# Optimization experiments

Measured on AMD Instinct MI355X. Metric: run time of the kernel, lower is better.

Reference implementation:

```python
import jax, jax.numpy as jnp
import numpy as np

N = 50000       # node_num
E = 800000      # edges (no self loops; reference adds them)
IN_C = 128
OUT_C = 128
HEADS = 1
NEG_SLOPE = 0.2
BN_EPS = 1e-5


def setup_inputs() -> dict:
    key = jax.random.key(0)
    ks = jax.random.split(key, 12)
    x = jax.random.normal(ks[0], (N, IN_C), dtype=jnp.float32)
    # edge_index with no self-loops: dst = (src + off) % N, off in [1, N)
    src = jax.random.randint(ks[1], (E,), 0, N)
    off = jax.random.randint(ks[2], (E,), 1, N)
    dst = (src + off) % N
    edge_index = jnp.stack([src, dst]).astype(jnp.int64)
    embedding = jax.random.normal(ks[3], (N, OUT_C), dtype=jnp.float32)
    s = 1.0 / np.sqrt(IN_C)
    lin_w = jax.random.uniform(ks[4], (HEADS * OUT_C, IN_C), jnp.float32, -s, s)
    g = 0.1
    att_i = jax.random.normal(ks[5], (1, HEADS, OUT_C), jnp.float32) * g
    att_j = jax.random.normal(ks[6], (1, HEADS, OUT_C), jnp.float32) * g
    att_em_i = jax.random.normal(ks[7], (1, HEADS, OUT_C), jnp.float32) * g
    att_em_j = jax.random.normal(ks[8], (1, HEADS, OUT_C), jnp.float32) * g
    bias = jnp.zeros((OUT_C,), jnp.float32)
    gamma = jnp.ones((OUT_C,), jnp.float32)
    beta = jnp.zeros((OUT_C,), jnp.float32)
    return {"x": x, "edge_index": edge_index, "embedding": embedding,
            "lin_w": lin_w, "att_i": att_i, "att_j": att_j,
            "att_em_i": att_em_i, "att_em_j": att_em_j,
            "bias": bias, "gamma": gamma, "beta": beta}


def _gnn_forward(x, embedding, lin_w, att_i, att_j, att_em_i, att_em_j,
                 bias, gamma, beta, src, dst):
    n = x.shape[0]
    xl = (x @ lin_w.T).reshape(n, HEADS, OUT_C)          # [N,H,C]
    x_j = xl[src]                                         # [E',H,C] source
    x_i = xl[dst]                                         # [E',H,C] target
    emb_i = embedding[dst][:, None, :]                    # [E',1,C]
    emb_j = embedding[src][:, None, :]
    # alpha_e = <[x_i||emb_i], [att_i||att_em_i]> + <[x_j||emb_j], [att_j||att_em_j]>
    alpha = ((x_i * att_i).sum(-1) + (emb_i * att_em_i).sum(-1)
             + (x_j * att_j).sum(-1) + (emb_j * att_em_j).sum(-1))  # [E',H]
    alpha = jnp.where(alpha >= 0, alpha, NEG_SLOPE * alpha)         # leaky_relu
    # segment softmax over destination node (PyG softmax)
    amax = jax.ops.segment_max(alpha, dst, num_segments=n)
    ex = jnp.exp(alpha - amax[dst])
    denom = jax.ops.segment_sum(ex, dst, num_segments=n)
    alpha = ex / (denom[dst] + 1e-16)                               # [E',H]
    out = jax.ops.segment_sum(x_j * alpha[..., None], dst, num_segments=n)  # [N,H,C]
    out = out.mean(axis=1) + bias                                   # concat=False
    # BatchNorm1d, training mode (biased batch variance)
    mu = out.mean(axis=0)
    var = ((out - mu) ** 2).mean(axis=0)
    return (out - mu) * jax.lax.rsqrt(var + BN_EPS) * gamma + beta


def reference(x, edge_index, embedding, lin_w, att_i, att_j,
              att_em_i, att_em_j, bias, gamma, beta):
    n = x.shape[0]
    loops = jnp.arange(n, dtype=edge_index.dtype)
    src = jnp.concatenate([edge_index[0], loops])
    dst = jnp.concatenate([edge_index[1], loops])
    return _gnn_forward(x, embedding, lin_w, att_i, att_j, att_em_i,
                        att_em_j, bias, gamma, beta, src, dst)
```

## Files before the change

kernel.cpp:

```cpp
#include <hip/hip_runtime.h>

typedef short bf16x8 __attribute__((ext_vector_type(8)));
typedef float f32x4 __attribute__((ext_vector_type(4)));

__device__ __forceinline__ unsigned short f2bf(float f) {
  unsigned int u = __float_as_uint(f);
  u += 0x7fffu + ((u >> 16) & 1u);
  return (unsigned short)(u >> 16);
}
__device__ __forceinline__ float bf2f(unsigned short h) {
  return __uint_as_float(((unsigned int)h) << 16);
}
__device__ __forceinline__ float lrelu(float a) { return a >= 0.f ? a : 0.2f * a; }

__global__ void zero_kernel(int* __restrict__ p, int n) {
  int i = blockIdx.x * blockDim.x + threadIdx.x;
  int stride = gridDim.x * blockDim.x;
  for (; i < n; i += stride) p[i] = 0;
}

__global__ __launch_bounds__(256) void gemm_kernel(
    const float* __restrict__ x, const float* __restrict__ w,
    unsigned short* __restrict__ xl, int n) {
  __shared__ __align__(16) unsigned short xs[64 * 128];
  __shared__ __align__(16) unsigned short wl[128 * 128];
  const int t = threadIdx.x;
  const int r0 = blockIdx.x * 64;
#pragma unroll
  for (int i = 0; i < 16; ++i) {
    int f4 = t + i * 256;
    int row = f4 >> 5;
    int kk = (f4 & 31) << 2;
    float4 v = *(const float4*)(w + row * 128 + kk);
    ushort4 b;
    b.x = f2bf(v.x); b.y = f2bf(v.y); b.z = f2bf(v.z); b.w = f2bf(v.w);
    int boff = (kk << 1) ^ ((row & 7) << 4);
    *(ushort4*)((char*)wl + row * 256 + boff) = b;
  }
#pragma unroll
  for (int i = 0; i < 8; ++i) {
    int f4 = t + i * 256;
    int row = f4 >> 5;
    int kk = (f4 & 31) << 2;
    int gr = r0 + row;
    float4 v;
    if (gr < n) v = *(const float4*)(x + gr * 128 + kk);
    else { v.x = 0.f; v.y = 0.f; v.z = 0.f; v.w = 0.f; }
    ushort4 b;
    b.x = f2bf(v.x); b.y = f2bf(v.y); b.z = f2bf(v.z); b.w = f2bf(v.w);
    int boff = (kk << 1) ^ ((row & 7) << 4);
    *(ushort4*)((char*)xs + row * 256 + boff) = b;
  }
  __syncthreads();
  const int wid = t >> 6, lane = t & 63;
  const int m16 = lane & 15, kg = lane >> 4;
  const int arow = wid * 16 + m16;
  const f32x4 vzero = {0.f, 0.f, 0.f, 0.f};
  f32x4 acc[8];
#pragma unroll
  for (int i = 0; i < 8; ++i) acc[i] = vzero;
#pragma unroll
  for (int s = 0; s < 4; ++s) {
    int kb = s * 64 + kg * 16;
    bf16x8 a = *(const bf16x8*)((const char*)xs + arow * 256 + (kb ^ ((arow & 7) << 4)));
#pragma unroll
    for (int cf = 0; cf < 8; ++cf) {
      int wrow = cf * 16 + m16;
      bf16x8 b = *(const bf16x8*)((const char*)wl + wrow * 256 + (kb ^ ((wrow & 7) << 4)));
      acc[cf] = __builtin_amdgcn_mfma_f32_16x16x32_bf16(a, b, acc[cf], 0, 0, 0);
    }
  }
  const int crow0 = wid * 16 + (lane >> 4) * 4;
#pragma unroll
  for (int q = 0; q < 4; ++q) {
    int gr = r0 + crow0 + q;
    if (gr < n) {
#pragma unroll
      for (int cf = 0; cf < 8; ++cf)
        xl[gr * 128 + cf * 16 + m16] = f2bf(acc[cf][q]);
    }
  }
}

__global__ __launch_bounds__(256) void atts_kernel(
    const unsigned short* __restrict__ xl, const float* __restrict__ emb,
    const float* __restrict__ att_i, const float* __restrict__ att_j,
    const float* __restrict__ att_em_i, const float* __restrict__ att_em_j,
    float* __restrict__ ai, float* __restrict__ aj, int n) {
  int wid = threadIdx.x >> 6, lane = threadIdx.x & 63;
  int node = blockIdx.x * 4 + wid;
  if (node >= n) return;
  int c0 = lane, c1 = lane + 64;
  float x0 = bf2f(xl[node * 128 + c0]);
  float x1 = bf2f(xl[node * 128 + c1]);
  float e0 = emb[node * 128 + c0];
  float e1 = emb[node * 128 + c1];
  float si = x0 * att_i[c0] + x1 * att_i[c1] + e0 * att_em_i[c0] + e1 * att_em_i[c1];
  float sj = x0 * att_j[c0] + x1 * att_j[c1] + e0 * att_em_j[c0] + e1 * att_em_j[c1];
#pragma unroll
  for (int off = 32; off > 0; off >>= 1) {
    si += __shfl_xor(si, off);
    sj += __shfl_xor(sj, off);
  }
  if (lane == 0) { ai[node] = si; aj[node] = sj; }
}

__global__ __launch_bounds__(256) void count_rank_kernel(
    const int* __restrict__ dst, int* __restrict__ cnt, int* __restrict__ pw, int E) {
  int e = (blockIdx.x * blockDim.x + threadIdx.x) * 4;
  if (e + 3 < E) {
    int4 d4 = *(const int4*)(dst + e);
    int4 p4;
    p4.x = atomicAdd(&cnt[d4.x], 1);
    p4.y = atomicAdd(&cnt[d4.y], 1);
    p4.z = atomicAdd(&cnt[d4.z], 1);
    p4.w = atomicAdd(&cnt[d4.w], 1);
    *(int4*)(pw + e) = p4;
  } else {
    for (; e < E; ++e) pw[e] = atomicAdd(&cnt[dst[e]], 1);
  }
}

__global__ __launch_bounds__(1024) void scan1_kernel(
    const int* __restrict__ cnt, int* __restrict__ rp, int* __restrict__ bsum, int n) {
  __shared__ int wsum[16];
  int t = threadIdx.x, lane = t & 63, wid = t >> 6;
  int i = blockIdx.x * 1024 + t;
  int v = (i < n) ? cnt[i] : 0;
  int incl = v;
#pragma unroll
  for (int off = 1; off < 64; off <<= 1) {
    int u = __shfl_up(incl, off);
    if (lane >= off) incl += u;
  }
  if (lane == 63) wsum[wid] = incl;
  __syncthreads();
  if (t < 16) {
    int wv = wsum[t];
    int winc = wv;
#pragma unroll
    for (int off = 1; off < 16; off <<= 1) {
      int u = __shfl_up(winc, off);
      if (t >= off) winc += u;
    }
    wsum[t] = winc - wv;
  }
  __syncthreads();
  int excl = wsum[wid] + incl - v;
  if (i < n) rp[i] = excl;
  if (t == 1023) bsum[blockIdx.x] = excl + v;
}

__global__ __launch_bounds__(64) void scan2_kernel(
    int* __restrict__ bsum, int* __restrict__ rp, int nb, int n) {
  int t = threadIdx.x;
  int carry = 0;
  for (int base = 0; base < nb; base += 64) {
    int idx = base + t;
    int v = (idx < nb) ? bsum[idx] : 0;
    int incl = v;
#pragma unroll
    for (int off = 1; off < 64; off <<= 1) {
      int u = __shfl_up(incl, off);
      if (t >= off) incl += u;
    }
    if (idx < nb) bsum[idx] = carry + incl - v;
    carry += __shfl(incl, 63);
  }
  if (t == 0) rp[n] = carry;
}

__global__ __launch_bounds__(256) void scan3_kernel(
    const int* __restrict__ bsum, int* __restrict__ rp, int n) {
  int i = blockIdx.x * blockDim.x + threadIdx.x;
  if (i < n) rp[i] += bsum[i >> 10];
}

__global__ __launch_bounds__(256) void scatter_kernel(
    const int* __restrict__ src, const int* __restrict__ dst,
    const int* __restrict__ rp, const int* __restrict__ pw,
    int* __restrict__ csr, int E) {
  int e = (blockIdx.x * blockDim.x + threadIdx.x) * 4;
  if (e + 3 < E) {
    int4 s4 = *(const int4*)(src + e);
    int4 d4 = *(const int4*)(dst + e);
    int4 p4 = *(const int4*)(pw + e);
    int r0 = rp[d4.x], r1 = rp[d4.y], r2 = rp[d4.z], r3 = rp[d4.w];
    csr[r0 + p4.x] = s4.x;
    csr[r1 + p4.y] = s4.y;
    csr[r2 + p4.z] = s4.z;
    csr[r3 + p4.w] = s4.w;
  } else {
    for (; e < E; ++e) csr[rp[dst[e]] + pw[e]] = src[e];
  }
}

__global__ __launch_bounds__(256) void agg_kernel(
    const float* __restrict__ ai, const float* __restrict__ aj,
    const unsigned short* __restrict__ xl,
    const int* __restrict__ row_ptr, const int* __restrict__ csr_src,
    const float* __restrict__ bias, float* __restrict__ out, int n) {
  __shared__ float s_we[4][64];
  __shared__ int s_id[4][64];
  int wid = threadIdx.x >> 6, lane = threadIdx.x & 63;
  int node = blockIdx.x * 4 + wid;
  if (node >= n) return;
  int beg = row_ptr[node], end = row_ptr[node + 1];
  float ain = ai[node];
  float a_self = lrelu(ain + aj[node]);
  float m = a_self;
  float dl = 0.f;
  float acc0 = 0.f, acc1 = 0.f;
  const int c0 = lane * 2;
  for (int cs = beg; cs < end; cs += 64) {
    int ce = min(64, end - cs);
    int s = 0;
    float a = -3.4e38f;
    if (lane < ce) {
      s = csr_src[cs + lane];
      a = lrelu(ain + aj[s]);
    }
    float cm = a;
#pragma unroll
    for (int off = 32; off > 0; off >>= 1) cm = fmaxf(cm, __shfl_xor(cm, off));
    float nm = fmaxf(m, cm);
    float scale = __expf(m - nm);
    dl *= scale; acc0 *= scale; acc1 *= scale;
    m = nm;
    float we = (lane < ce) ? __expf(a - nm) : 0.f;
    dl += we;
    s_we[wid][lane] = we;
    s_id[wid][lane] = s;
    int j = 0;
    for (; j + 4 <= ce; j += 4) {
      float w0 = s_we[wid][j],     w1 = s_we[wid][j + 1];
      float w2 = s_we[wid][j + 2], w3 = s_we[wid][j + 3];
      int i0 = s_id[wid][j],     i1 = s_id[wid][j + 1];
      int i2 = s_id[wid][j + 2], i3 = s_id[wid][j + 3];
      ushort2 v0 = *(const ushort2*)(xl + i0 * 128 + c0);
      ushort2 v1 = *(const ushort2*)(xl + i1 * 128 + c0);
      ushort2 v2 = *(const ushort2*)(xl + i2 * 128 + c0);
      ushort2 v3 = *(const ushort2*)(xl + i3 * 128 + c0);
      acc0 += w0 * bf2f(v0.x); acc1 += w0 * bf2f(v0.y);
      acc0 += w1 * bf2f(v1.x); acc1 += w1 * bf2f(v1.y);
      acc0 += w2 * bf2f(v2.x); acc1 += w2 * bf2f(v2.y);
      acc0 += w3 * bf2f(v3.x); acc1 += w3 * bf2f(v3.y);
    }
    for (; j < ce; ++j) {
      float w0 = s_we[wid][j];
      int i0 = s_id[wid][j];
      ushort2 v0 = *(const ushort2*)(xl + i0 * 128 + c0);
      acc0 += w0 * bf2f(v0.x); acc1 += w0 * bf2f(v0.y);
    }
  }
  float w_self = __expf(a_self - m);
#pragma unroll
  for (int off = 32; off > 0; off >>= 1) dl += __shfl_xor(dl, off);
  float inv = 1.f / (dl + w_self + 1e-16f);
  ushort2 u = *(const ushort2*)(xl + node * 128 + c0);
  float2 o;
  o.x = (acc0 + w_self * bf2f(u.x)) * inv + bias[c0];
  o.y = (acc1 + w_self * bf2f(u.y)) * inv + bias[c0 + 1];
  *(float2*)(out + node * 128 + c0) = o;
}

__global__ __launch_bounds__(256) void bnstat_kernel(
    const float* __restrict__ out, float* __restrict__ sums,
    float* __restrict__ sumsq, int n) {
  int c = threadIdx.x & 127;
  int half = threadIdx.x >> 7;
  float s = 0.f, q = 0.f;
  for (int r = blockIdx.x * 2 + half; r < n; r += gridDim.x * 2) {
    float v = out[r * 128 + c];
    s += v;
    q += v * v;
  }
  atomicAdd(&sums[c], s);
  atomicAdd(&sumsq[c], q);
}

__global__ __launch_bounds__(256) void bnapply_kernel(
    float* __restrict__ out, const float* __restrict__ sums,
    const float* __restrict__ sumsq, const float* __restrict__ gamma,
    const float* __restrict__ beta, int n, float invN) {
  int total = n * 128;
  int i = blockIdx.x * blockDim.x + threadIdx.x;
  int stride = gridDim.x * blockDim.x;
  for (; i < total; i += stride) {
    int c = i & 127;
    float mu = sums[c] * invN;
    float var = sumsq[c] * invN - mu * mu;
    out[i] = (out[i] - mu) * rsqrtf(var + 1e-5f) * gamma[c] + beta[c];
  }
}

extern "C" void kernel_launch(void* const* d_in, const int* in_sizes, int n_in,
                              void* d_out, int out_size, void* d_ws, size_t ws_size,
                              hipStream_t stream) {
  (void)n_in; (void)out_size; (void)ws_size;
  const float* x = (const float*)d_in[0];
  const int* ei = (const int*)d_in[1];
  const float* emb = (const float*)d_in[2];
  const float* lin_w = (const float*)d_in[3];
  const float* att_i = (const float*)d_in[4];
  const float* att_j = (const float*)d_in[5];
  const float* att_em_i = (const float*)d_in[6];
  const float* att_em_j = (const float*)d_in[7];
  const float* bias = (const float*)d_in[8];
  const float* gamma = (const float*)d_in[9];
  const float* beta = (const float*)d_in[10];
  float* out = (float*)d_out;
  const int N = in_sizes[0] / 128;
  const int E = in_sizes[1] / 2;
  const int* src = ei;
  const int* dst = ei + E;
  const int NB = (N + 1023) / 1024;

  auto align_up = [](size_t v) { return (v + 255) & ~(size_t)255; };
  size_t off = 0;
  size_t xl_off = off;    off = align_up(off + (size_t)N * 128 * 2);
  size_t ai_off = off;    off = align_up(off + (size_t)N * 4);
  size_t aj_off = off;    off = align_up(off + (size_t)N * 4);
  size_t rp_off = off;    off = align_up(off + (size_t)(N + 1) * 4);
  size_t csr_off = off;   off = align_up(off + (size_t)E * 4);
  size_t pw_off = off;    off = align_up(off + (size_t)E * 4);
  size_t bsum_off = off;  off = align_up(off + (size_t)(NB + 1) * 4);
  size_t cnt_off = off;   off = align_up(off + (size_t)N * 4);
  size_t sums_off = off;  off = align_up(off + 512);
  size_t sumsq_off = off; off = align_up(off + 512);
  size_t end_off = off;

  char* ws = (char*)d_ws;
  unsigned short* xl = (unsigned short*)(ws + xl_off);
  float* ai = (float*)(ws + ai_off);
  float* aj = (float*)(ws + aj_off);
  int* rp = (int*)(ws + rp_off);
  int* csr = (int*)(ws + csr_off);
  int* pw = (int*)(ws + pw_off);
  int* bsum = (int*)(ws + bsum_off);
  int* cnt = (int*)(ws + cnt_off);
  float* sums = (float*)(ws + sums_off);
  float* sumsq = (float*)(ws + sumsq_off);

  int zwords = (int)((end_off - cnt_off) / 4);
  hipLaunchKernelGGL(zero_kernel, dim3((zwords + 255) / 256), dim3(256), 0, stream,
                     cnt, zwords);
  hipLaunchKernelGGL(gemm_kernel, dim3((N + 63) / 64), dim3(256), 0, stream,
                     x, lin_w, xl, N);
  hipLaunchKernelGGL(atts_kernel, dim3((N + 3) / 4), dim3(256), 0, stream,
                     xl, emb, att_i, att_j, att_em_i, att_em_j, ai, aj, N);
  hipLaunchKernelGGL(count_rank_kernel, dim3((E / 4 + 255) / 256), dim3(256), 0, stream,
                     dst, cnt, pw, E);
  hipLaunchKernelGGL(scan1_kernel, dim3(NB), dim3(1024), 0, stream, cnt, rp, bsum, N);
  hipLaunchKernelGGL(scan2_kernel, dim3(1), dim3(64), 0, stream, bsum, rp, NB, N);
  hipLaunchKernelGGL(scan3_kernel, dim3((N + 255) / 256), dim3(256), 0, stream,
                     bsum, rp, N);
  hipLaunchKernelGGL(scatter_kernel, dim3((E / 4 + 255) / 256), dim3(256), 0, stream,
                     src, dst, rp, pw, csr, E);
  hipLaunchKernelGGL(agg_kernel, dim3((N + 3) / 4), dim3(256), 0, stream,
                     ai, aj, xl, rp, csr, bias, out, N);
  hipLaunchKernelGGL(bnstat_kernel, dim3(256), dim3(256), 0, stream,
                     out, sums, sumsq, N);
  hipLaunchKernelGGL(bnapply_kernel, dim3(2048), dim3(256), 0, stream,
                     out, sums, sumsq, gamma, beta, N, 1.0f / (float)N);
}
```

Before: 262.8 us.

## Fuse attention scores into GEMM, drop softmax max, vectorize BN kernels

Several changes at once. The per-node attention dot products move into the GEMM epilogue, computed from the MFMA accumulators plus a vectorized embedding read, which removes the separate atts kernel and its reread of xl. The aggregation kernel drops the online running-max softmax and exponentiates the raw leaky-relu scores. It also passes edge weights and indices through wave shuffles instead of LDS and unrolls the gather by 8. The BatchNorm stat and apply kernels switch to float4 accesses, with a block-level LDS reduction and precomputed scale and shift. Skipping the max subtraction risks exp overflow when attention logits are large.

```diff
diff --git a/kernel.cpp b/kernel.cpp
--- a/kernel.cpp
+++ b/kernel.cpp
@@ -21,7 +21,11 @@
 
 __global__ __launch_bounds__(256) void gemm_kernel(
     const float* __restrict__ x, const float* __restrict__ w,
-    unsigned short* __restrict__ xl, int n) {
+    const float* __restrict__ emb,
+    const float* __restrict__ att_i, const float* __restrict__ att_j,
+    const float* __restrict__ att_em_i, const float* __restrict__ att_em_j,
+    unsigned short* __restrict__ xl, float* __restrict__ ai, float* __restrict__ aj,
+    int n) {
   __shared__ __align__(16) unsigned short xs[64 * 128];
   __shared__ __align__(16) unsigned short wl[128 * 128];
   const int t = threadIdx.x;
@@ -70,7 +74,7 @@
       acc[cf] = __builtin_amdgcn_mfma_f32_16x16x32_bf16(a, b, acc[cf], 0, 0, 0);
     }
   }
-  const int crow0 = wid * 16 + (lane >> 4) * 4;
+  const int crow0 = wid * 16 + kg * 4;
 #pragma unroll
   for (int q = 0; q < 4; ++q) {
     int gr = r0 + crow0 + q;
@@ -80,29 +84,41 @@
         xl[gr * 128 + cf * 16 + m16] = f2bf(acc[cf][q]);
     }
   }
-}
-
-__global__ __launch_bounds__(256) void atts_kernel(
-    const unsigned short* __restrict__ xl, const float* __restrict__ emb,
-    const float* __restrict__ att_i, const float* __restrict__ att_j,
-    const float* __restrict__ att_em_i, const float* __restrict__ att_em_j,
-    float* __restrict__ ai, float* __restrict__ aj, int n) {
-  int wid = threadIdx.x >> 6, lane = threadIdx.x & 63;
-  int node = blockIdx.x * 4 + wid;
-  if (node >= n) return;
-  int c0 = lane, c1 = lane + 64;
-  float x0 = bf2f(xl[node * 128 + c0]);
-  float x1 = bf2f(xl[node * 128 + c1]);
-  float e0 = emb[node * 128 + c0];
-  float e1 = emb[node * 128 + c1];
-  float si = x0 * att_i[c0] + x1 * att_i[c1] + e0 * att_em_i[c0] + e1 * att_em_i[c1];
-  float sj = x0 * att_j[c0] + x1 * att_j[c1] + e0 * att_em_j[c0] + e1 * att_em_j[c1];
-#pragma unroll
-  for (int off = 32; off > 0; off >>= 1) {
-    si += __shfl_xor(si, off);
-    sj += __shfl_xor(sj, off);
-  }
-  if (lane == 0) { ai[node] = si; aj[node] = sj; }
+  float ati[8], atj[8];
+#pragma unroll
+  for (int cf = 0; cf < 8; ++cf) {
+    ati[cf] = att_i[cf * 16 + m16];
+    atj[cf] = att_j[cf * 16 + m16];
+  }
+  float4 aemi0 = *(const float4*)(att_em_i + m16 * 8);
+  float4 aemi1 = *(const float4*)(att_em_i + m16 * 8 + 4);
+  float4 aemj0 = *(const float4*)(att_em_j + m16 * 8);
+  float4 aemj1 = *(const float4*)(att_em_j + m16 * 8 + 4);
+#pragma unroll
+  for (int q = 0; q < 4; ++q) {
+    int gr = r0 + crow0 + q;
+    if (gr < n) {
+      float si = 0.f, sj = 0.f;
+#pragma unroll
+      for (int cf = 0; cf < 8; ++cf) {
+        si += acc[cf][q] * ati[cf];
+        sj += acc[cf][q] * atj[cf];
+      }
+      const float* ep = emb + (size_t)gr * 128 + m16 * 8;
+      float4 e0 = *(const float4*)(ep);
+      float4 e1 = *(const float4*)(ep + 4);
+      si += e0.x * aemi0.x + e0.y * aemi0.y + e0.z * aemi0.z + e0.w * aemi0.w
+          + e1.x * aemi1.x + e1.y * aemi1.y + e1.z * aemi1.z + e1.w * aemi1.w;
+      sj += e0.x * aemj0.x + e0.y * aemj0.y + e0.z * aemj0.z + e0.w * aemj0.w
+          + e1.x * aemj1.x + e1.y * aemj1.y + e1.z * aemj1.z + e1.w * aemj1.w;
+#pragma unroll
+      for (int off = 1; off < 16; off <<= 1) {
+        si += __shfl_xor(si, off);
+        sj += __shfl_xor(sj, off);
+      }
+      if (m16 == 0) { ai[gr] = si; aj[gr] = sj; }
+    }
+  }
 }
 
 __global__ __launch_bounds__(256) void count_rank_kernel(
@@ -200,97 +216,129 @@
     const unsigned short* __restrict__ xl,
     const int* __restrict__ row_ptr, const int* __restrict__ csr_src,
     const float* __restrict__ bias, float* __restrict__ out, int n) {
-  __shared__ float s_we[4][64];
-  __shared__ int s_id[4][64];
   int wid = threadIdx.x >> 6, lane = threadIdx.x & 63;
   int node = blockIdx.x * 4 + wid;
   if (node >= n) return;
   int beg = row_ptr[node], end = row_ptr[node + 1];
   float ain = ai[node];
-  float a_self = lrelu(ain + aj[node]);
-  float m = a_self;
+  float w_self = __expf(lrelu(ain + aj[node]));
   float dl = 0.f;
   float acc0 = 0.f, acc1 = 0.f;
   const int c0 = lane * 2;
   for (int cs = beg; cs < end; cs += 64) {
     int ce = min(64, end - cs);
     int s = 0;
-    float a = -3.4e38f;
+    float we = 0.f;
     if (lane < ce) {
       s = csr_src[cs + lane];
-      a = lrelu(ain + aj[s]);
-    }
-    float cm = a;
-#pragma unroll
-    for (int off = 32; off > 0; off >>= 1) cm = fmaxf(cm, __shfl_xor(cm, off));
-    float nm = fmaxf(m, cm);
-    float scale = __expf(m - nm);
-    dl *= scale; acc0 *= scale; acc1 *= scale;
-    m = nm;
-    float we = (lane < ce) ? __expf(a - nm) : 0.f;
+      we = __expf(lrelu(ain + aj[s]));
+    }
     dl += we;
-    s_we[wid][lane] = we;
-    s_id[wid][lane] = s;
     int j = 0;
-    for (; j + 4 <= ce; j += 4) {
-      float w0 = s_we[wid][j],     w1 = s_we[wid][j + 1];
-      float w2 = s_we[wid][j + 2], w3 = s_we[wid][j + 3];
-      int i0 = s_id[wid][j],     i1 = s_id[wid][j + 1];
-      int i2 = s_id[wid][j + 2], i3 = s_id[wid][j + 3];
-      ushort2 v0 = *(const ushort2*)(xl + i0 * 128 + c0);
-      ushort2 v1 = *(const ushort2*)(xl + i1 * 128 + c0);
-      ushort2 v2 = *(const ushort2*)(xl + i2 * 128 + c0);
-      ushort2 v3 = *(const ushort2*)(xl + i3 * 128 + c0);
+    for (; j + 8 <= ce; j += 8) {
+      float w0 = __shfl(we, j),     w1 = __shfl(we, j + 1);
+      float w2 = __shfl(we, j + 2), w3 = __shfl(we, j + 3);
+      float w4 = __shfl(we, j + 4), w5 = __shfl(we, j + 5);
+      float w6 = __shfl(we, j + 6), w7 = __shfl(we, j + 7);
+      int i0 = __shfl(s, j),     i1 = __shfl(s, j + 1);
+      int i2 = __shfl(s, j + 2), i3 = __shfl(s, j + 3);
+      int i4 = __shfl(s, j + 4), i5 = __shfl(s, j + 5);
+      int i6 = __shfl(s, j + 6), i7 = __shfl(s, j + 7);
+      ushort2 v0 = *(const ushort2*)(xl + (size_t)i0 * 128 + c0);
+      ushort2 v1 = *(const ushort2*)(xl + (size_t)i1 * 128 + c0);
+      ushort2 v2 = *(const ushort2*)(xl + (size_t)i2 * 128 + c0);
+      ushort2 v3 = *(const ushort2*)(xl + (size_t)i3 * 128 + c0);
+      ushort2 v4 = *(const ushort2*)(xl + (size_t)i4 * 128 + c0);
+      ushort2 v5 = *(const ushort2*)(xl + (size_t)i5 * 128 + c0);
+      ushort2 v6 = *(const ushort2*)(xl + (size_t)i6 * 128 + c0);
+      ushort2 v7 = *(const ushort2*)(xl + (size_t)i7 * 128 + c0);
       acc0 += w0 * bf2f(v0.x); acc1 += w0 * bf2f(v0.y);
       acc0 += w1 * bf2f(v1.x); acc1 += w1 * bf2f(v1.y);
       acc0 += w2 * bf2f(v2.x); acc1 += w2 * bf2f(v2.y);
       acc0 += w3 * bf2f(v3.x); acc1 += w3 * bf2f(v3.y);
+      acc0 += w4 * bf2f(v4.x); acc1 += w4 * bf2f(v4.y);
+      acc0 += w5 * bf2f(v5.x); acc1 += w5 * bf2f(v5.y);
+      acc0 += w6 * bf2f(v6.x); acc1 += w6 * bf2f(v6.y);
+      acc0 += w7 * bf2f(v7.x); acc1 += w7 * bf2f(v7.y);
     }
     for (; j < ce; ++j) {
-      float w0 = s_we[wid][j];
-      int i0 = s_id[wid][j];
-      ushort2 v0 = *(const ushort2*)(xl + i0 * 128 + c0);
-      acc0 += w0 * bf2f(v0.x); acc1 += w0 * bf2f(v0.y);
-    }
-  }
-  float w_self = __expf(a_self - m);
+      float wj = __shfl(we, j);
+      int ij = __shfl(s, j);
+      ushort2 v = *(const ushort2*)(xl + (size_t)ij * 128 + c0);
+      acc0 += wj * bf2f(v.x); acc1 += wj * bf2f(v.y);
+    }
+  }
 #pragma unroll
   for (int off = 32; off > 0; off >>= 1) dl += __shfl_xor(dl, off);
   float inv = 1.f / (dl + w_self + 1e-16f);
-  ushort2 u = *(const ushort2*)(xl + node * 128 + c0);
+  ushort2 u = *(const ushort2*)(xl + (size_t)node * 128 + c0);
   float2 o;
   o.x = (acc0 + w_self * bf2f(u.x)) * inv + bias[c0];
   o.y = (acc1 + w_self * bf2f(u.y)) * inv + bias[c0 + 1];
-  *(float2*)(out + node * 128 + c0) = o;
+  *(float2*)(out + (size_t)node * 128 + c0) = o;
 }
 
 __global__ __launch_bounds__(256) void bnstat_kernel(
     const float* __restrict__ out, float* __restrict__ sums,
     float* __restrict__ sumsq, int n) {
-  int c = threadIdx.x & 127;
-  int half = threadIdx.x >> 7;
-  float s = 0.f, q = 0.f;
-  for (int r = blockIdx.x * 2 + half; r < n; r += gridDim.x * 2) {
-    float v = out[r * 128 + c];
-    s += v;
-    q += v * v;
-  }
-  atomicAdd(&sums[c], s);
-  atomicAdd(&sumsq[c], q);
+  __shared__ float4 red_s[8][32];
+  __shared__ float4 red_q[8][32];
+  int q = threadIdx.x & 31;
+  int rs = threadIdx.x >> 5;
+  float4 s = {0.f, 0.f, 0.f, 0.f}, ss = {0.f, 0.f, 0.f, 0.f};
+  for (int r = blockIdx.x * 8 + rs; r < n; r += gridDim.x * 8) {
+    float4 v = *(const float4*)(out + (size_t)r * 128 + q * 4);
+    s.x += v.x; s.y += v.y; s.z += v.z; s.w += v.w;
+    ss.x += v.x * v.x; ss.y += v.y * v.y; ss.z += v.z * v.z; ss.w += v.w * v.w;
+  }
+  red_s[rs][q] = s;
+  red_q[rs][q] = ss;
+  __syncthreads();
+  if (threadIdx.x < 32) {
+    float4 ts = red_s[0][threadIdx.x], tq = red_q[0][threadIdx.x];
+#pragma unroll
+    for (int k = 1; k < 8; ++k) {
+      float4 a = red_s[k][threadIdx.x], b = red_q[k][threadIdx.x];
+      ts.x += a.x; ts.y += a.y; ts.z += a.z; ts.w += a.w;
+      tq.x += b.x; tq.y += b.y; tq.z += b.z; tq.w += b.w;
+    }
+    int c = threadIdx.x * 4;
+    atomicAdd(&sums[c + 0], ts.x); atomicAdd(&sums[c + 1], ts.y);
+    atomicAdd(&sums[c + 2], ts.z); atomicAdd(&sums[c + 3], ts.w);
+    atomicAdd(&sumsq[c + 0], tq.x); atomicAdd(&sumsq[c + 1], tq.y);
+    atomicAdd(&sumsq[c + 2], tq.z); atomicAdd(&sumsq[c + 3], tq.w);
+  }
 }
 
 __global__ __launch_bounds__(256) void bnapply_kernel(
     float* __restrict__ out, const float* __restrict__ sums,
     const float* __restrict__ sumsq, const float* __restrict__ gamma,
     const float* __restrict__ beta, int n, float invN) {
-  int total = n * 128;
-  int i = blockIdx.x * blockDim.x + threadIdx.x;
-  int stride = gridDim.x * blockDim.x;
-  for (; i < total; i += stride) {
-    int c = i & 127;
-    float mu = sums[c] * invN;
-    float var = sumsq[c] * invN - mu * mu;
-    out[i] = (out[i] - mu) * rsqrtf(var + 1e-5f) * gamma[c] + beta[c];
+  int q = threadIdx.x & 31;
+  int rs = threadIdx.x >> 5;
+  int c = q * 4;
+  float4 mu, var, sc, sh;
+  mu.x = sums[c + 0] * invN; mu.y = sums[c + 1] * invN;
+  mu.z = sums[c + 2] * invN; mu.w = sums[c + 3] * invN;
+  var.x = sumsq[c + 0] * invN - mu.x * mu.x;
+  var.y = sumsq[c + 1] * invN - mu.y * mu.y;
+  var.z = sumsq[c + 2] * invN - mu.z * mu.z;
+  var.w = sumsq[c + 3] * invN - mu.w * mu.w;
+  sc.x = rsqrtf(var.x + 1e-5f) * gamma[c + 0];
+  sc.y = rsqrtf(var.y + 1e-5f) * gamma[c + 1];
+  sc.z = rsqrtf(var.z + 1e-5f) * gamma[c + 2];
+  sc.w = rsqrtf(var.w + 1e-5f) * gamma[c + 3];
+  sh.x = beta[c + 0] - mu.x * sc.x;
+  sh.y = beta[c + 1] - mu.y * sc.y;
+  sh.z = beta[c + 2] - mu.z * sc.z;
+  sh.w = beta[c + 3] - mu.w * sc.w;
+  for (int r = blockIdx.x * 8 + rs; r < n; r += gridDim.x * 8) {
+    float4 v = *(const float4*)(out + (size_t)r * 128 + c);
+    v.x = v.x * sc.x + sh.x;
+    v.y = v.y * sc.y + sh.y;
+    v.z = v.z * sc.z + sh.z;
+    v.w = v.w * sc.w + sh.w;
+    *(float4*)(out + (size_t)r * 128 + c) = v;
   }
 }
 
@@ -346,9 +394,8 @@
   hipLaunchKernelGGL(zero_kernel, dim3((zwords + 255) / 256), dim3(256), 0, stream,
                      cnt, zwords);
   hipLaunchKernelGGL(gemm_kernel, dim3((N + 63) / 64), dim3(256), 0, stream,
-                     x, lin_w, xl, N);
-  hipLaunchKernelGGL(atts_kernel, dim3((N + 3) / 4), dim3(256), 0, stream,
-                     xl, emb, att_i, att_j, att_em_i, att_em_j, ai, aj, N);
+                     x, lin_w, emb, att_i, att_j, att_em_i, att_em_j,
+                     xl, ai, aj, N);
   hipLaunchKernelGGL(count_rank_kernel, dim3((E / 4 + 255) / 256), dim3(256), 0, stream,
                      dst, cnt, pw, E);
   hipLaunchKernelGGL(scan1_kernel, dim3(NB), dim3(1024), 0, stream, cnt, rp, bsum, N);
@@ -359,7 +406,7 @@
                      src, dst, rp, pw, csr, E);
   hipLaunchKernelGGL(agg_kernel, dim3((N + 3) / 4), dim3(256), 0, stream,
                      ai, aj, xl, rp, csr, bias, out, N);
-  hipLaunchKernelGGL(bnstat_kernel, dim3(256), dim3(256), 0, stream,
+  hipLaunchKernelGGL(bnstat_kernel, dim3(512), dim3(256), 0, stream,
                      out, sums, sumsq, N);
   hipLaunchKernelGGL(bnapply_kernel, dim3(2048), dim3(256), 0, stream,
                      out, sums, sumsq, gamma, beta, N, 1.0f / (float)N);
```

Result: slower. 280.5 us (+6.7%).
